# Optimization experiments

Hardware: AMD Instinct MI355X
Metric: run time of the kernel (lower is better)

## Reference

```python
import jax, jax.numpy as jnp
import numpy as np

B, S0, S1 = 4, 768, 256
T = S0 + S1
W0, W1 = 2048, 1024
N, K, H = 8, 1, 256  # num_heads, num_kv_heads (MQA), head_dim
G = N // K
MAX_WAVELENGTH = 10000.0
BIG_NEG = -2.3819763e+38


def _apply_rope(x, positions):
    """RoPE: positions [B,L] applied to x [B,L,heads,H]."""
    half = x.shape[-1] // 2
    freq_exponents = (2.0 / x.shape[-1]) * jnp.arange(half, dtype=jnp.float32)
    timescale = MAX_WAVELENGTH ** freq_exponents  # [half]
    radians = positions[..., None].astype(jnp.float32) / timescale  # [B,L,half]
    radians = radians[..., None, :]  # [B,L,1,half]
    sin, cos = jnp.sin(radians), jnp.cos(radians)
    x1, x2 = jnp.split(x.astype(jnp.float32), 2, axis=-1)
    res = jnp.concatenate([x1 * cos - x2 * sin, x2 * cos + x1 * sin], axis=-1)
    return res.astype(x.dtype)


def setup_inputs() -> dict:
    key = jax.random.key(0)
    ks = jax.random.split(key, 8)
    x0 = jax.random.normal(ks[0], (B, S0, W0), dtype=jnp.float32)
    x1 = jax.random.normal(ks[1], (B, S1, W1), dtype=jnp.float32)
    positions = jnp.broadcast_to(jnp.arange(T, dtype=jnp.int32)[None, :], (B, T))
    # causal mask [B,1,T,T]
    attn_mask = jnp.broadcast_to(jnp.tril(jnp.ones((T, T), dtype=bool))[None, None], (B, 1, T, T))
    # lecun_normal on the width (in) axis
    q0_w = jax.random.normal(ks[2], (N, W0, H), dtype=jnp.float32) / np.sqrt(W0)
    kv0_w = jax.random.normal(ks[3], (2, K, W0, H), dtype=jnp.float32) / np.sqrt(W0)
    out0_w = jax.random.normal(ks[4], (N, H, W0), dtype=jnp.float32) / np.sqrt(N * H)
    q1_w = jax.random.normal(ks[5], (N, W1, H), dtype=jnp.float32) / np.sqrt(W1)
    kv1_w = jax.random.normal(ks[6], (2, K, W1, H), dtype=jnp.float32) / np.sqrt(W1)
    out1_w = jax.random.normal(ks[7], (N, H, W1), dtype=jnp.float32) / np.sqrt(N * H)
    return {"x0": x0, "x1": x1, "positions": positions, "attn_mask": attn_mask,
            "q0_w": q0_w, "kv0_w": kv0_w, "out0_w": out0_w,
            "q1_w": q1_w, "kv1_w": kv1_w, "out1_w": out1_w}


def reference(x0, x1, positions, attn_mask, q0_w, kv0_w, out0_w, q1_w, kv1_w, out1_w):
    dtype = x0.dtype
    # per-modality QKV projections (num_kv_heads != num_heads branch)
    q0 = jnp.einsum('BTD,NDH->BTNH', x0, q0_w.astype(dtype))
    k0, v0 = jnp.einsum('BSD,2KDH->2BSKH', x0, kv0_w.astype(dtype))
    q1 = jnp.einsum('BTD,NDH->BTNH', x1, q1_w.astype(dtype))
    k1, v1 = jnp.einsum('BSD,2KDH->2BSKH', x1, kv1_w.astype(dtype))
    q = jnp.concatenate([q0, q1], axis=1)  # [B,T,N,H]
    k = jnp.concatenate([k0, k1], axis=1)  # [B,T,K,H]
    v = jnp.concatenate([v0, v1], axis=1)
    q = _apply_rope(q, positions) * (H ** -0.5)
    k = _apply_rope(k, positions)
    # prefill cache init: cache_size == attn_mask.shape[-1] == T, so no padding
    idx = jnp.full((B,), T, dtype=jnp.int32)
    # GQA attention
    qg = q.reshape(B, T, K, G, H)  # 'B T (K G) H -> B T K G H'
    logits = jnp.einsum('BTKGH,BSKH->BKGTS', qg, k, preferred_element_type=jnp.float32)
    masked = jnp.where(attn_mask[:, :, None, :, :], logits, BIG_NEG)
    probs = jax.nn.softmax(masked, axis=-1).astype(dtype)
    enc = jnp.einsum('BKGTS,BSKH->BTKGH', probs, v).reshape(B, T, N, H)
    out0 = jnp.einsum('BTNH,NHD->BTD', enc[:, :S0], out0_w.astype(dtype))
    out1 = jnp.einsum('BTNH,NHD->BTD', enc[:, S0:], out1_w.astype(dtype))
    return (out0, out1, idx, k, v)
```

## Files before the change

kernel.cpp:

```cpp
#include <hip/hip_runtime.h>

typedef unsigned short u16;
typedef __attribute__((ext_vector_type(8))) short short8;
typedef __attribute__((ext_vector_type(4))) float f32x4;
typedef __attribute__((ext_vector_type(4))) unsigned short u16x4;

__device__ __forceinline__ u16 f2bf(float f){
  unsigned u = __float_as_uint(f);
  u += 0x7FFFu + ((u >> 16) & 1u);
  return (u16)(u >> 16);
}
__device__ __forceinline__ float bf2f(u16 h){
  return __uint_as_float(((unsigned)h) << 16);
}
__device__ __forceinline__ void gload16(const void* g, void* l){
  __builtin_amdgcn_global_load_lds((const __attribute__((address_space(1))) void*)g,
                                   (__attribute__((address_space(3))) void*)l, 16, 0, 0);
}
__device__ __forceinline__ f32x4 mfma16(short8 a, short8 b, f32x4 c){
  return __builtin_amdgcn_mfma_f32_16x16x32_bf16(a, b, c, 0, 0, 0);
}
__device__ __forceinline__ short8 ld8(const u16* p){
  return *reinterpret_cast<const short8*>(p);
}
__device__ __forceinline__ unsigned cvtpk(float lo, float hi){
  unsigned r;
  asm volatile("v_cvt_pk_bf16_f32 %0, %1, %2" : "=v"(r) : "v"(lo), "v"(hi));
  return r;
}

__device__ __forceinline__
void transp_body(const float* __restrict__ S, u16* __restrict__ D,
                 int K, int C, int kb, int cb){
  __shared__ float t[32][33];
  int tx = threadIdx.x & 31, ty = threadIdx.x >> 5;
  #pragma unroll
  for (int i = ty; i < 32; i += 8)
    t[i][tx] = S[(size_t)(kb + i) * C + cb + tx];
  __syncthreads();
  #pragma unroll
  for (int i = ty; i < 32; i += 8)
    D[(size_t)(cb + i) * K + kb + tx] = f2bf(t[tx][i]);
}
__global__ __launch_bounds__(256)
void prep_all(const float* __restrict__ x0, const float* __restrict__ x1,
              u16* __restrict__ x0b, u16* __restrict__ x1b,
              const float* q0_w, const float* kv0_w, const float* q1_w,
              const float* kv1_w, const float* o0_w, const float* o1_w,
              u16* qkv0T, u16* qkv1T, u16* o0T, u16* o1T){
  int bid = blockIdx.x;
  if (bid < 7168){
    const float* s; u16* d; int i;
    if (bid < 6144){ s = x0; d = x0b; i = bid * 256 + threadIdx.x; }
    else           { s = x1; d = x1b; i = (bid - 6144) * 256 + threadIdx.x; }
    float4 v = reinterpret_cast<const float4*>(s)[i];
    u16x4 o = { f2bf(v.x), f2bf(v.y), f2bf(v.z), f2bf(v.w) };
    reinterpret_cast<u16x4*>(d)[i] = o;
    return;
  }
  bid -= 7168;
  const float* S; u16* D; int K, C, nkc, lid;
  if (bid < 4096){
    S = q0_w; D = qkv0T; K = 2048; C = 256; lid = bid;
  } else if (bid < 5120){
    S = kv0_w; D = qkv0T + (size_t)2048*2048; K = 2048; C = 256; lid = bid - 4096;
  } else if (bid < 7168){
    S = q1_w; D = qkv1T; K = 1024; C = 256; lid = bid - 5120;
  } else if (bid < 7680){
    S = kv1_w; D = qkv1T + (size_t)2048*1024; K = 1024; C = 256; lid = bid - 7168;
  } else if (bid < 11776){
    S = o0_w; D = o0T; K = 2048; C = 2048; lid = bid - 7680;
  } else {
    S = o1_w; D = o1T; K = 2048; C = 1024; lid = bid - 11776;
  }
  nkc = (K >> 5) * (C >> 5);
  int z   = lid / nkc;
  int rem = lid - z * nkc;
  int kb  = (rem / (C >> 5)) << 5;
  int cb  = (rem % (C >> 5)) << 5;
  transp_body(S + (size_t)z * K * C, D + (size_t)z * K * C, K, C, kb, cb);
}

__device__ __forceinline__
void gemm_body(const u16* __restrict__ A, int lda, int aS, int aT, int aOff,
               const u16* __restrict__ BT, int ldbt,
               u16* __restrict__ Cb, float* __restrict__ Cf, int ldc,
               int cS, int cT, int cOff, int N, int Kd, int bid, char* smem){
  int ntx = N >> 7;
  int bm = bid / ntx;
  int bn = bid - bm * ntx;
  int row0 = bm << 7, col0 = bn << 7;
  size_t arow0 = (size_t)(row0 / aS) * aT + (row0 % aS) + aOff;
  size_t crow0 = (size_t)(row0 / cS) * cT + (row0 % cS) + cOff;
  const u16* Abase = A + arow0 * (size_t)lda;
  const u16* Bbase = BT + (size_t)col0 * ldbt;
  int tid = threadIdx.x;
  int w = tid >> 6, l = tid & 63;
  int wr = (w >> 1) << 6, wc = (w & 1) << 6;
  int lr = l & 15, g4 = l >> 4, lq = (l >> 4) << 2;
  int keyr = lr & 7;
  f32x4 acc[4][4];
  #pragma unroll
  for (int m = 0; m < 4; m++)
    #pragma unroll
    for (int n = 0; n < 4; n++)
      acc[m][n] = (f32x4){0.f, 0.f, 0.f, 0.f};
  int scol = (((tid & 7) ^ ((tid >> 3) & 7)) << 3);
  const u16* gA = Abase + (size_t)(tid >> 3) * lda + scol;
  const u16* gB = Bbase + (size_t)(tid >> 3) * ldbt + scol;
  int dsto = tid * 16;

  auto STAGE = [&](char* dst, int k0){
    gload16(gA + k0,                      dst + dsto);
    gload16(gA + (size_t)32*lda  + k0,    dst + 4096  + dsto);
    gload16(gA + (size_t)64*lda  + k0,    dst + 8192  + dsto);
    gload16(gA + (size_t)96*lda  + k0,    dst + 12288 + dsto);
    gload16(gB + k0,                      dst + 16384 + dsto);
    gload16(gB + (size_t)32*ldbt + k0,    dst + 20480 + dsto);
    gload16(gB + (size_t)64*ldbt + k0,    dst + 24576 + dsto);
    gload16(gB + (size_t)96*ldbt + k0,    dst + 28672 + dsto);
  };

  STAGE(smem, 0);
  int cur = 0;
  for (int k0 = 0; k0 < Kd; k0 += 64, cur ^= 1){
    asm volatile("" ::: "memory");
    __builtin_amdgcn_s_barrier();
    asm volatile("" ::: "memory");
    if (k0 + 64 < Kd){
      STAGE(smem + (cur ^ 1) * 32768, k0 + 64);
      asm volatile("s_waitcnt vmcnt(8)" ::: "memory");
    } else {
      asm volatile("s_waitcnt vmcnt(0)" ::: "memory");
    }
    __builtin_amdgcn_s_barrier();
    asm volatile("" ::: "memory");
    const u16* As = (const u16*)(smem + cur * 32768);
    const u16* Bs = As + 8192;
    #pragma unroll
    for (int kk = 0; kk < 2; kk++){
      int so = ((g4 + kk*4) ^ keyr) << 3;
      short8 af[4], bfr[4];
      #pragma unroll
      for (int m = 0; m < 4; m++)
        af[m] = ld8(&As[(wr + m*16 + lr)*64 + so]);
      #pragma unroll
      for (int n = 0; n < 4; n++)
        bfr[n] = ld8(&Bs[(wc + n*16 + lr)*64 + so]);
      #pragma unroll
      for (int m = 0; m < 4; m++)
        #pragma unroll
        for (int n = 0; n < 4; n++)
          acc[m][n] = mfma16(af[m], bfr[n], acc[m][n]);
    }
  }
  #pragma unroll
  for (int m = 0; m < 4; m++){
    #pragma unroll
    for (int i = 0; i < 4; i++){
      size_t r = crow0 + wr + m*16 + lq + i;
      if (Cb){
        #pragma unroll
        for (int n = 0; n < 4; n++)
          Cb[r*ldc + col0 + wc + n*16 + lr] = f2bf(acc[m][n][i]);
      } else {
        #pragma unroll
        for (int n = 0; n < 4; n++)
          Cf[r*ldc + col0 + wc + n*16 + lr] = acc[m][n][i];
      }
    }
  }
}

__global__ __launch_bounds__(256)
void gemm_qkv(const u16* __restrict__ x0b, const u16* __restrict__ qkv0T,
              const u16* __restrict__ x1b, const u16* __restrict__ qkv1T,
              u16* __restrict__ qkvb){
  extern __shared__ __align__(16) char smem[];
  int bid = blockIdx.x;
  if (bid < 480)
    gemm_body(x0b, 2048, 3072, 3072, 0, qkv0T, 2048,
              qkvb, nullptr, 2560, 768, 1024, 0, 2560, 2048, bid, smem);
  else
    gemm_body(x1b, 1024, 1024, 1024, 0, qkv1T, 1024,
              qkvb, nullptr, 2560, 256, 1024, 768, 2560, 1024, bid - 480, smem);
}

__global__ __launch_bounds__(256)
void gemm_out(const u16* __restrict__ encb, const u16* __restrict__ o0T,
              const u16* __restrict__ o1T, float* __restrict__ out0,
              float* __restrict__ out1){
  extern __shared__ __align__(16) char smem[];
  int bid = blockIdx.x;
  if (bid < 384)
    gemm_body(encb, 2048, 768, 1024, 0, o0T, 2048,
              nullptr, out0, 2048, 3072, 3072, 0, 2048, 2048, bid, smem);
  else
    gemm_body(encb, 2048, 256, 1024, 768, o1T, 2048,
              nullptr, out1, 1024, 1024, 1024, 0, 1024, 2048, bid - 384, smem);
}

__global__ void rope_kernel(u16* __restrict__ qkv, const int* __restrict__ positions,
                            float* __restrict__ k_out, float* __restrict__ v_out,
                            float* __restrict__ idx_out){
  int bt = blockIdx.x;
  int j = threadIdx.x;
  float pos = (float)positions[bt];
  float ts = powf(10000.0f, (float)j * 0.0078125f);
  float rad = pos / ts;
  float sn, cs;
  sincosf(rad, &sn, &cs);
  u16* q = qkv + (size_t)bt * 2560;
  #pragma unroll
  for (int n = 0; n < 8; n++){
    float x1 = bf2f(q[n*256 + j]);
    float x2 = bf2f(q[n*256 + 128 + j]);
    q[n*256 + j]       = f2bf((x1*cs - x2*sn) * 0.0625f);
    q[n*256 + 128 + j] = f2bf((x2*cs + x1*sn) * 0.0625f);
  }
  u16* kv = q + 2048;
  float x1 = bf2f(kv[j]), x2 = bf2f(kv[128 + j]);
  float k1 = x1*cs - x2*sn, k2 = x2*cs + x1*sn;
  kv[j] = f2bf(k1); kv[128 + j] = f2bf(k2);
  size_t ko = (size_t)bt * 256;
  k_out[ko + j] = k1;  k_out[ko + 128 + j] = k2;
  v_out[ko + j] = bf2f(kv[256 + j]);
  v_out[ko + 128 + j] = bf2f(kv[384 + j]);
  if (bt == 0 && j < 4) idx_out[j] = 1024.0f;
}

__global__ void transpose_v(const u16* __restrict__ qkv, u16* __restrict__ vT){
  __shared__ u16 t[32][33];
  int b = blockIdx.z;
  int tb = blockIdx.x * 32, hb = blockIdx.y * 32;
  int tx = threadIdx.x, ty = threadIdx.y;
  #pragma unroll
  for (int i = ty; i < 32; i += 8)
    t[i][tx] = qkv[(size_t)(b*1024 + tb + i)*2560 + 2304 + hb + tx];
  __syncthreads();
  #pragma unroll
  for (int i = ty; i < 32; i += 8)
    vT[(size_t)(b*256 + hb + i)*1024 + tb + tx] = t[tx][i];
}

__global__ __launch_bounds__(256, 2)
void attn_kernel(const u16* __restrict__ qkv, const u16* __restrict__ vT,
                 u16* __restrict__ enc){
  extern __shared__ __align__(16) char smem[];
  int bid = blockIdx.x;
  int b   = bid & 3;
  int h2  = (bid >> 2) & 1;
  int qt  = 63 - (bid >> 3);
  int tid = threadIdx.x;
  int w = tid >> 6;
  int head = h2*4 + w;
  int l = tid & 63;
  int lr = l & 15;
  int g = l >> 4;
  int lkqe  = g << 3;
  int lkq16 = g << 4;
  int q0 = qt << 4, nkv = q0 + 16;
  int swk = (lr & 7) << 4;
  int swv = ((lr >> 1) & 3) << 4;

  const char* kbase = (const char*)qkv + (size_t)b*5242880 + 4096;
  const char* vbase = (const char*)vT + (size_t)b*524288;
  const char* ksrc[4]; const char* vsrc[4];
  int kldo[4], vldo[4];
  #pragma unroll
  for (int r = 0; r < 4; r++){
    int o = r*4096 + tid*16;
    int krow = o >> 9;
    int kcol = (o & 511) ^ ((krow & 7) << 4);
    ksrc[r] = kbase + (size_t)krow*5120 + kcol;
    kldo[r] = o;
    int vrow = o >> 6;
    int vcol = (o & 63) ^ (((vrow >> 1) & 3) << 4);
    vsrc[r] = vbase + (size_t)vrow*2048 + vcol;
    vldo[r] = 16384 + o;
  }

  const u16* qb = qkv + ((size_t)(b*1024 + q0)) * 2560 + head*256;
  short8 qf[8];
  #pragma unroll
  for (int hf = 0; hf < 8; hf++)
    qf[hf] = ld8(qb + (size_t)lr*2560 + hf*32 + lkqe);

  f32x4 o_[16];
  #pragma unroll
  for (int hf = 0; hf < 16; hf++)
    o_[hf] = (f32x4){0.f,0.f,0.f,0.f};
  float mrow = -3.0e38f, lrow = 0.f;

  auto STAGE = [&](int buf, int kt){
    char* dst = smem + buf*32768;
    #pragma unroll
    for (int r = 0; r < 4; r++)
      gload16(ksrc[r] + (size_t)kt*5120, dst + kldo[r]);
    #pragma unroll
    for (int r = 0; r < 4; r++)
      gload16(vsrc[r] + (size_t)kt*2, dst + vldo[r]);
  };

  STAGE(0, 0);
  int cur = 0;
  for (int kt = 0; kt < nkv; kt += 32, cur ^= 1){
    asm volatile("" ::: "memory");
    __builtin_amdgcn_s_barrier();
    asm volatile("" ::: "memory");
    if (kt + 32 < nkv){
      STAGE(cur ^ 1, kt + 32);
      asm volatile("s_waitcnt vmcnt(8)" ::: "memory");
    } else {
      asm volatile("s_waitcnt vmcnt(0)" ::: "memory");
    }
    __builtin_amdgcn_s_barrier();
    asm volatile("" ::: "memory");

    const char* Kb = smem + cur*32768;
    const char* Vb = Kb + 16384;
    f32x4 s[2];
    s[0] = (f32x4){0.f,0.f,0.f,0.f};
    s[1] = (f32x4){0.f,0.f,0.f,0.f};
    __builtin_amdgcn_s_setprio(1);
    #pragma unroll
    for (int hf = 0; hf < 8; hf++){
      int colb = (hf*64 + lkq16) ^ swk;
      short8 k0 = *(const short8*)(Kb + (size_t)(lr     )*512 + colb);
      short8 k1 = *(const short8*)(Kb + (size_t)(lr + 16)*512 + colb);
      s[0] = mfma16(k0, qf[hf], s[0]);
      s[1] = mfma16(k1, qf[hf], s[1]);
    }
    __builtin_amdgcn_s_setprio(0);
    if (kt + 32 > q0){
      #pragma unroll
      for (int cf = 0; cf < 2; cf++)
        #pragma unroll
        for (int i = 0; i < 4; i++){
          int kv_g = kt + cf*16 + g*4 + i;
          if (kv_g > q0 + lr) s[cf][i] = -1.0e30f;
        }
    }
    float m8 = fmaxf(fmaxf(fmaxf(s[0][0], s[0][1]), fmaxf(s[0][2], s[0][3])),
                     fmaxf(fmaxf(s[1][0], s[1][1]), fmaxf(s[1][2], s[1][3])));
    m8 = fmaxf(m8, __shfl_xor(m8, 16, 64));
    m8 = fmaxf(m8, __shfl_xor(m8, 32, 64));
    bool nd = (m8 > mrow + 8.f);
    if (__ballot(nd)){
      float mn = fmaxf(mrow, m8);
      float corr = __expf(mrow - mn);
      mrow = mn;
      lrow *= corr;
      #pragma unroll
      for (int hf = 0; hf < 16; hf++)
        #pragma unroll
        for (int i = 0; i < 4; i++)
          o_[hf][i] *= corr;
    }
    float p[2][4];
    #pragma unroll
    for (int cf = 0; cf < 2; cf++)
      #pragma unroll
      for (int i = 0; i < 4; i++)
        p[cf][i] = __expf(s[cf][i] - mrow);
    float sum8 = p[0][0] + p[0][1] + p[0][2] + p[0][3]
               + p[1][0] + p[1][1] + p[1][2] + p[1][3];
    sum8 += __shfl_xor(sum8, 16, 64);
    sum8 += __shfl_xor(sum8, 32, 64);
    lrow += sum8;
    unsigned A0 = cvtpk(p[0][0], p[0][1]);
    unsigned A1 = cvtpk(p[0][2], p[0][3]);
    unsigned B0 = cvtpk(p[1][0], p[1][1]);
    unsigned B1 = cvtpk(p[1][2], p[1][3]);
    unsigned sp0 = (unsigned)__shfl_xor((int)(g < 2 ? A0 : B0), 16, 64);
    unsigned sp1 = (unsigned)__shfl_xor((int)(g < 2 ? A1 : B1), 16, 64);
    unsigned c0  = (unsigned)__shfl_xor((int)(l < 32 ? B0 : A0), 32, 64);
    unsigned c1  = (unsigned)__shfl_xor((int)(l < 32 ? B1 : A1), 32, 64);
    unsigned pc0 = (unsigned)__shfl_xor((int)c0, 16, 64);
    unsigned pc1 = (unsigned)__shfl_xor((int)c1, 16, 64);
    union { unsigned u[4]; short8 v; } pf;
    pf.u[0] = (g == 0) ? A0 : (g == 1) ? pc0 : (g == 2) ? c0  : sp0;
    pf.u[1] = (g == 0) ? A1 : (g == 1) ? pc1 : (g == 2) ? c1  : sp1;
    pf.u[2] = (g == 0) ? sp0 : (g == 1) ? c0 : (g == 2) ? pc0 : B0;
    pf.u[3] = (g == 0) ? sp1 : (g == 1) ? c1 : (g == 2) ? pc1 : B1;
    __builtin_amdgcn_s_setprio(1);
    #pragma unroll
    for (int hf = 0; hf < 16; hf++){
      const char* vr = Vb + (size_t)(hf*16 + lr)*64;
      short8 v0 = *(const short8*)(vr + (lkq16 ^ swv));
      o_[hf] = mfma16(v0, pf.v, o_[hf]);
    }
    __builtin_amdgcn_s_setprio(0);
  }
  u16* eb = enc + ((size_t)(b*1024 + q0 + lr)) * 2048 + head*256;
  float inv = 1.0f / lrow;
  #pragma unroll
  for (int hf = 0; hf < 16; hf++){
    u16x4 st = { f2bf(o_[hf][0] * inv), f2bf(o_[hf][1] * inv),
                 f2bf(o_[hf][2] * inv), f2bf(o_[hf][3] * inv) };
    *reinterpret_cast<u16x4*>(eb + hf*16 + g*4) = st;
  }
}

extern "C" void kernel_launch(void* const* d_in, const int* in_sizes, int n_in,
                              void* d_out, int out_size, void* d_ws, size_t ws_size,
                              hipStream_t stream){
  const float* x0     = (const float*)d_in[0];
  const float* x1     = (const float*)d_in[1];
  const int*   pos    = (const int*)d_in[2];
  const float* q0_w   = (const float*)d_in[4];
  const float* kv0_w  = (const float*)d_in[5];
  const float* out0_w = (const float*)d_in[6];
  const float* q1_w   = (const float*)d_in[7];
  const float* kv1_w  = (const float*)d_in[8];
  const float* out1_w = (const float*)d_in[9];

  float* out  = (float*)d_out;
  float* out0 = out;
  float* out1 = out + 6291456;
  float* idxp = out + 7340032;
  float* kout = out + 7340036;
  float* vout = out + 8388612;

  char* ws = (char*)d_ws;
  size_t off = 0;
  auto alloc = [&](size_t bytes){
    void* p = ws + off;
    off = (off + bytes + 255) & ~(size_t)255;
    return p;
  };
  u16* x0b   = (u16*)alloc((size_t)6291456 * 2);
  u16* x1b   = (u16*)alloc((size_t)1048576 * 2);
  u16* qkv0T = (u16*)alloc((size_t)2560 * 2048 * 2);
  u16* qkv1T = (u16*)alloc((size_t)2560 * 1024 * 2);
  u16* o0T   = (u16*)alloc((size_t)2048 * 2048 * 2);
  u16* o1T   = (u16*)alloc((size_t)1024 * 2048 * 2);
  u16* qkvb  = (u16*)alloc((size_t)4096 * 2560 * 2);
  u16* vTb   = (u16*)alloc((size_t)4 * 256 * 1024 * 2);
  u16* encb  = (u16*)alloc((size_t)4096 * 2048 * 2);

  hipFuncSetAttribute((const void*)attn_kernel,
                      hipFuncAttributeMaxDynamicSharedMemorySize, 65536);
  hipFuncSetAttribute((const void*)gemm_qkv,
                      hipFuncAttributeMaxDynamicSharedMemorySize, 65536);
  hipFuncSetAttribute((const void*)gemm_out,
                      hipFuncAttributeMaxDynamicSharedMemorySize, 65536);

  prep_all<<<20992, 256, 0, stream>>>(x0, x1, x0b, x1b,
                                      q0_w, kv0_w, q1_w, kv1_w, out0_w, out1_w,
                                      qkv0T, qkv1T, o0T, o1T);

  gemm_qkv<<<640, 256, 65536, stream>>>(x0b, qkv0T, x1b, qkv1T, qkvb);

  rope_kernel<<<4096, 128, 0, stream>>>(qkvb, pos, kout, vout, idxp);
  transpose_v<<<dim3(32, 8, 4), dim3(32,8), 0, stream>>>(qkvb, vTb);
  attn_kernel<<<512, 256, 65536, stream>>>(qkvb, vTb, encb);

  gemm_out<<<448, 256, 65536, stream>>>(encb, o0T, o1T, out0, out1);
}
```

Measured before the change: 164.5 us.

## Use single-barrier double buffering, fuse rope with V transpose, defer softmax reductions

The GEMM and attention loops now wait for all outstanding loads and use one barrier per iteration instead of two. They then issue the next tile's loads into the other buffer, which keeps the copy overlapped with compute. The rope and V-transpose kernels are merged into one launch with block-range dispatch, saving a kernel launch. In attention, the cross-lane max reduction only runs when the ballot shows a rescale is needed, and the row-sum shuffle reduction is moved out of the loop to the epilogue. The cost is a full vmcnt(0) wait at the top of each iteration, which could expose load latency if compute per tile is short.

```diff
diff --git a/kernel.cpp b/kernel.cpp
--- a/kernel.cpp
+++ b/kernel.cpp
@@ -124,17 +124,11 @@
   STAGE(smem, 0);
   int cur = 0;
   for (int k0 = 0; k0 < Kd; k0 += 64, cur ^= 1){
-    asm volatile("" ::: "memory");
+    asm volatile("s_waitcnt vmcnt(0)" ::: "memory");
     __builtin_amdgcn_s_barrier();
     asm volatile("" ::: "memory");
-    if (k0 + 64 < Kd){
+    if (k0 + 64 < Kd)
       STAGE(smem + (cur ^ 1) * 32768, k0 + 64);
-      asm volatile("s_waitcnt vmcnt(8)" ::: "memory");
-    } else {
-      asm volatile("s_waitcnt vmcnt(0)" ::: "memory");
-    }
-    __builtin_amdgcn_s_barrier();
-    asm volatile("" ::: "memory");
     const u16* As = (const u16*)(smem + cur * 32768);
     const u16* Bs = As + 8192;
     #pragma unroll
@@ -200,40 +194,46 @@
               nullptr, out1, 1024, 1024, 1024, 0, 1024, 2048, bid - 384, smem);
 }
 
-__global__ void rope_kernel(u16* __restrict__ qkv, const int* __restrict__ positions,
-                            float* __restrict__ k_out, float* __restrict__ v_out,
-                            float* __restrict__ idx_out){
-  int bt = blockIdx.x;
-  int j = threadIdx.x;
-  float pos = (float)positions[bt];
-  float ts = powf(10000.0f, (float)j * 0.0078125f);
-  float rad = pos / ts;
-  float sn, cs;
-  sincosf(rad, &sn, &cs);
-  u16* q = qkv + (size_t)bt * 2560;
-  #pragma unroll
-  for (int n = 0; n < 8; n++){
-    float x1 = bf2f(q[n*256 + j]);
-    float x2 = bf2f(q[n*256 + 128 + j]);
-    q[n*256 + j]       = f2bf((x1*cs - x2*sn) * 0.0625f);
-    q[n*256 + 128 + j] = f2bf((x2*cs + x1*sn) * 0.0625f);
-  }
-  u16* kv = q + 2048;
-  float x1 = bf2f(kv[j]), x2 = bf2f(kv[128 + j]);
-  float k1 = x1*cs - x2*sn, k2 = x2*cs + x1*sn;
-  kv[j] = f2bf(k1); kv[128 + j] = f2bf(k2);
-  size_t ko = (size_t)bt * 256;
-  k_out[ko + j] = k1;  k_out[ko + 128 + j] = k2;
-  v_out[ko + j] = bf2f(kv[256 + j]);
-  v_out[ko + 128 + j] = bf2f(kv[384 + j]);
-  if (bt == 0 && j < 4) idx_out[j] = 1024.0f;
-}
-
-__global__ void transpose_v(const u16* __restrict__ qkv, u16* __restrict__ vT){
+__global__ __launch_bounds__(256)
+void rope_tv(u16* __restrict__ qkv, const int* __restrict__ positions,
+             float* __restrict__ k_out, float* __restrict__ v_out,
+             float* __restrict__ idx_out, u16* __restrict__ vT){
+  int bid = blockIdx.x;
+  int tid = threadIdx.x;
+  if (bid < 2048){
+    int bt = bid*2 + (tid >> 7);
+    int j = tid & 127;
+    float pos = (float)positions[bt];
+    float ts = powf(10000.0f, (float)j * 0.0078125f);
+    float rad = pos / ts;
+    float sn, cs;
+    sincosf(rad, &sn, &cs);
+    u16* q = qkv + (size_t)bt * 2560;
+    #pragma unroll
+    for (int n = 0; n < 8; n++){
+      float x1 = bf2f(q[n*256 + j]);
+      float x2 = bf2f(q[n*256 + 128 + j]);
+      q[n*256 + j]       = f2bf((x1*cs - x2*sn) * 0.0625f);
+      q[n*256 + 128 + j] = f2bf((x2*cs + x1*sn) * 0.0625f);
+    }
+    u16* kv = q + 2048;
+    float x1 = bf2f(kv[j]), x2 = bf2f(kv[128 + j]);
+    float k1 = x1*cs - x2*sn, k2 = x2*cs + x1*sn;
+    kv[j] = f2bf(k1); kv[128 + j] = f2bf(k2);
+    size_t ko = (size_t)bt * 256;
+    k_out[ko + j] = k1;  k_out[ko + 128 + j] = k2;
+    v_out[ko + j] = bf2f(kv[256 + j]);
+    v_out[ko + 128 + j] = bf2f(kv[384 + j]);
+    if (bt == 0 && j < 4 && tid < 128) idx_out[j] = 1024.0f;
+    return;
+  }
   __shared__ u16 t[32][33];
-  int b = blockIdx.z;
-  int tb = blockIdx.x * 32, hb = blockIdx.y * 32;
-  int tx = threadIdx.x, ty = threadIdx.y;
+  int lid = bid - 2048;
+  int b = lid >> 8;
+  int rem = lid & 255;
+  int tb = (rem >> 3) << 5;
+  int hb = (rem & 7) << 5;
+  int tx = tid & 31, ty = tid >> 5;
   #pragma unroll
   for (int i = ty; i < 32; i += 8)
     t[i][tx] = qkv[(size_t)(b*1024 + tb + i)*2560 + 2304 + hb + tx];
@@ -305,17 +305,11 @@
   STAGE(0, 0);
   int cur = 0;
   for (int kt = 0; kt < nkv; kt += 32, cur ^= 1){
-    asm volatile("" ::: "memory");
+    asm volatile("s_waitcnt vmcnt(0)" ::: "memory");
     __builtin_amdgcn_s_barrier();
     asm volatile("" ::: "memory");
-    if (kt + 32 < nkv){
+    if (kt + 32 < nkv)
       STAGE(cur ^ 1, kt + 32);
-      asm volatile("s_waitcnt vmcnt(8)" ::: "memory");
-    } else {
-      asm volatile("s_waitcnt vmcnt(0)" ::: "memory");
-    }
-    __builtin_amdgcn_s_barrier();
-    asm volatile("" ::: "memory");
 
     const char* Kb = smem + cur*32768;
     const char* Vb = Kb + 16384;
@@ -341,12 +335,11 @@
           if (kv_g > q0 + lr) s[cf][i] = -1.0e30f;
         }
     }
-    float m8 = fmaxf(fmaxf(fmaxf(s[0][0], s[0][1]), fmaxf(s[0][2], s[0][3])),
+    float lm = fmaxf(fmaxf(fmaxf(s[0][0], s[0][1]), fmaxf(s[0][2], s[0][3])),
                      fmaxf(fmaxf(s[1][0], s[1][1]), fmaxf(s[1][2], s[1][3])));
-    m8 = fmaxf(m8, __shfl_xor(m8, 16, 64));
-    m8 = fmaxf(m8, __shfl_xor(m8, 32, 64));
-    bool nd = (m8 > mrow + 8.f);
-    if (__ballot(nd)){
+    if (__ballot(lm > mrow + 8.f)){
+      float m8 = fmaxf(lm, __shfl_xor(lm, 16, 64));
+      m8 = fmaxf(m8, __shfl_xor(m8, 32, 64));
       float mn = fmaxf(mrow, m8);
       float corr = __expf(mrow - mn);
       mrow = mn;
@@ -363,11 +356,8 @@
       #pragma unroll
       for (int i = 0; i < 4; i++)
         p[cf][i] = __expf(s[cf][i] - mrow);
-    float sum8 = p[0][0] + p[0][1] + p[0][2] + p[0][3]
-               + p[1][0] + p[1][1] + p[1][2] + p[1][3];
-    sum8 += __shfl_xor(sum8, 16, 64);
-    sum8 += __shfl_xor(sum8, 32, 64);
-    lrow += sum8;
+    lrow += p[0][0] + p[0][1] + p[0][2] + p[0][3]
+          + p[1][0] + p[1][1] + p[1][2] + p[1][3];
     unsigned A0 = cvtpk(p[0][0], p[0][1]);
     unsigned A1 = cvtpk(p[0][2], p[0][3]);
     unsigned B0 = cvtpk(p[1][0], p[1][1]);
@@ -392,6 +382,8 @@
     }
     __builtin_amdgcn_s_setprio(0);
   }
+  lrow += __shfl_xor(lrow, 16, 64);
+  lrow += __shfl_xor(lrow, 32, 64);
   u16* eb = enc + ((size_t)(b*1024 + q0 + lr)) * 2048 + head*256;
   float inv = 1.0f / lrow;
   #pragma unroll
@@ -452,8 +444,8 @@
 
   gemm_qkv<<<640, 256, 65536, stream>>>(x0b, qkv0T, x1b, qkv1T, qkvb);
 
-  rope_kernel<<<4096, 128, 0, stream>>>(qkvb, pos, kout, vout, idxp);
-  transpose_v<<<dim3(32, 8, 4), dim3(32,8), 0, stream>>>(qkvb, vTb);
+  rope_tv<<<3072, 256, 0, stream>>>(qkvb, pos, kout, vout, idxp, vTb);
+
   attn_kernel<<<512, 256, 65536, stream>>>(qkvb, vTb, encb);
 
   gemm_out<<<448, 256, 65536, stream>>>(encb, o0T, o1T, out0, out1);
```

After: 154.8 us. 1.06x faster.
